# Optimization experiments

Hardware: AMD Instinct MI355X
Metric: run time of the kernel (lower is better)

Reference implementation:

```python
import jax, jax.numpy as jnp
import numpy as np

B, S, D = 4, 4096, 1024   # batch, seq_len, hidden_dim
E, K = 8, 2               # num_experts, num_experts_per_tok
H = 2 * D                 # expert MLP hidden dim


def setup_inputs() -> dict:
    key = jax.random.key(0)
    ks = jax.random.split(key, 4)
    sc = 0.02
    return {
        "hidden_states": jax.random.normal(ks[0], (B, S, D), jnp.float32),
        "Wr": (jax.random.normal(ks[1], (D, E), jnp.float32) * sc),
        "br": jnp.zeros((E,), jnp.float32),
        "W1": (jax.random.normal(ks[2], (E, D, H), jnp.float32) * sc),
        "b1": jnp.zeros((E, H), jnp.float32),
        "W2": (jax.random.normal(ks[3], (E, H, D), jnp.float32) * sc),
        "b2": jnp.zeros((E, D), jnp.float32),
    }


def reference(hidden_states, Wr, br, W1, b1, W2, b2):
    # Router: Linear -> Softmax (over experts), then top-k on the probabilities
    probs = jax.nn.softmax(hidden_states @ Wr + br, axis=-1)          # [B,S,E]
    top_w, top_i = jax.lax.top_k(probs, K)                            # [B,S,K]
    top_w = top_w / (top_w.sum(axis=-1, keepdims=True) + 1e-8)
    # Per-expert combine weight for every token (0 if expert not in top-k)
    combine = (jax.nn.one_hot(top_i, E, dtype=top_w.dtype)
               * top_w[..., None]).sum(axis=-2)                       # [B,S,E]
    # Reference semantics: run EVERY expert on EVERY token, then mask
    h = jnp.einsum('bsd,edh->ebsh', hidden_states, W1) + b1[:, None, None, :]  # [E,B,S,H]
    h = jax.nn.gelu(h, approximate=False)                             # exact GELU (torch default)
    expert_out = jnp.einsum('ebsh,ehd->ebsd', h, W2) + b2[:, None, None, :]    # [E,B,S,D]
    output = jnp.einsum('ebsd,bse->bsd', expert_out, combine)         # [B,S,D]
    return output
```

## Files before the change

kernel.cpp:

```cpp
#include <hip/hip_runtime.h>
#include <hip/hip_bf16.h>
#include <cstdint>
#include <cstddef>

#define TOKENS 16384
#define DIM    1024
#define NEXP   8
#define HID    2048
#define PAIRS  32768
#define PADCAP 33792
#define MTILES 264

typedef short     bf16x8 __attribute__((ext_vector_type(8)));
typedef float     f32x4  __attribute__((ext_vector_type(4)));

__device__ __forceinline__ unsigned short f2bf(float f) {
  union { float f; uint32_t u; } v; v.f = f;
  uint32_t u = v.u;
  uint32_t r = (u + 0x7FFFu + ((u >> 16) & 1u)) >> 16;
  return (unsigned short)r;
}

__device__ __forceinline__ void gload_lds16(const void* g, void* l) {
  __builtin_amdgcn_global_load_lds(
      (const __attribute__((address_space(1))) unsigned int*)g,
      (__attribute__((address_space(3))) unsigned int*)l,
      16, 0, 0);
}

__global__ __launch_bounds__(256) void tcvt(const float* __restrict__ src,
                                            unsigned short* __restrict__ dst,
                                            int R, int C) {
  __shared__ unsigned short t[64][72];
  const float* s = src + (size_t)blockIdx.z * R * C;
  unsigned short* d = dst + (size_t)blockIdx.z * R * C;
  int r0 = blockIdx.y * 64, c0 = blockIdx.x * 64;
  int tr = threadIdx.x >> 4;
  int tc = threadIdx.x & 15;
#pragma unroll
  for (int i = 0; i < 4; ++i) {
    int r = tr + i * 16;
    float4 v = *(const float4*)&s[(size_t)(r0 + r) * C + c0 + tc * 4];
    t[r][tc * 4 + 0] = f2bf(v.x);
    t[r][tc * 4 + 1] = f2bf(v.y);
    t[r][tc * 4 + 2] = f2bf(v.z);
    t[r][tc * 4 + 3] = f2bf(v.w);
  }
  __syncthreads();
#pragma unroll
  for (int i = 0; i < 4; ++i) {
    int c = tr + i * 16;
    ushort4 o;
    o.x = t[tc * 4 + 0][c];
    o.y = t[tc * 4 + 1][c];
    o.z = t[tc * 4 + 2][c];
    o.w = t[tc * 4 + 3][c];
    *(ushort4*)&d[(size_t)(c0 + c) * R + r0 + tc * 4] = o;
  }
}

__global__ __launch_bounds__(256) void router(const float* __restrict__ hs,
                                              const float* __restrict__ Wr,
                                              const float* __restrict__ br,
                                              unsigned short* __restrict__ Xb,
                                              int2* __restrict__ tok_e,
                                              float2* __restrict__ tok_w,
                                              int* __restrict__ counts) {
  __shared__ float wrT[NEXP][1032];
  __shared__ int hist[NEXP];
  int tid = threadIdx.x;
  if (tid < NEXP) hist[tid] = 0;
#pragma unroll
  for (int j = 0; j < 4; ++j) {
    int d = tid * 4 + j;
    float4 lo = *(const float4*)&Wr[d * 8];
    float4 hi = *(const float4*)&Wr[d * 8 + 4];
    wrT[0][d] = lo.x; wrT[1][d] = lo.y; wrT[2][d] = lo.z; wrT[3][d] = lo.w;
    wrT[4][d] = hi.x; wrT[5][d] = hi.y; wrT[6][d] = hi.z; wrT[7][d] = hi.w;
  }
  __syncthreads();
  int wave = tid >> 6, lane = tid & 63;

  for (int i = 0; i < 4; ++i) {
    int t = blockIdx.x * 16 + wave * 4 + i;
    float4 x[4];
#pragma unroll
    for (int p = 0; p < 4; ++p) {
      int d = p * 256 + lane * 4;
      x[p] = *(const float4*)&hs[(size_t)t * DIM + d];
      ushort4 o;
      o.x = f2bf(x[p].x); o.y = f2bf(x[p].y); o.z = f2bf(x[p].z); o.w = f2bf(x[p].w);
      *(ushort4*)&Xb[(size_t)t * DIM + d] = o;
    }
    float acc[NEXP];
#pragma unroll
    for (int e = 0; e < NEXP; ++e) {
      float a = 0.f;
#pragma unroll
      for (int p = 0; p < 4; ++p) {
        float4 w4 = *(const float4*)&wrT[e][p * 256 + lane * 4];
        a += x[p].x * w4.x + x[p].y * w4.y + x[p].z * w4.z + x[p].w * w4.w;
      }
      acc[e] = a;
    }
#pragma unroll
    for (int e = 0; e < NEXP; ++e) {
#pragma unroll
      for (int off = 32; off; off >>= 1) acc[e] += __shfl_xor(acc[e], off);
    }
    if (lane == 0) {
      float l[NEXP];
#pragma unroll
      for (int e = 0; e < NEXP; ++e) l[e] = acc[e] + br[e];
      float m = l[0];
#pragma unroll
      for (int e = 1; e < NEXP; ++e) m = fmaxf(m, l[e]);
      float p[NEXP], s = 0.f;
#pragma unroll
      for (int e = 0; e < NEXP; ++e) { p[e] = expf(l[e] - m); s += p[e]; }
      int e0 = 0;
#pragma unroll
      for (int e = 1; e < NEXP; ++e) if (p[e] > p[e0]) e0 = e;
      int e1 = (e0 == 0) ? 1 : 0;
#pragma unroll
      for (int e = 0; e < NEXP; ++e) if (e != e0 && p[e] > p[e1]) e1 = e;
      float q0 = p[e0] / s, q1 = p[e1] / s;
      float den = q0 + q1 + 1e-8f;
      tok_e[t] = make_int2(e0, e1);
      tok_w[t] = make_float2(q0 / den, q1 / den);
      atomicAdd(&hist[e0], 1);
      atomicAdd(&hist[e1], 1);
    }
  }
  __syncthreads();
  if (tid < NEXP)
    atomicAdd(&counts[(tid * 8 + (blockIdx.x & 7)) * 32], hist[tid]);
}

__global__ void mk_offsets(const int* __restrict__ counts, int* __restrict__ offs) {
  __shared__ int tot[NEXP];
  int e = threadIdx.x;
  if (e < NEXP) {
    int c = 0;
#pragma unroll
    for (int p = 0; p < 8; ++p) c += counts[(e * 8 + p) * 32];
    tot[e] = c;
  }
  __syncthreads();
  if (threadIdx.x == 0) {
    int o = 0;
#pragma unroll
    for (int i = 0; i < NEXP; ++i) {
      offs[i] = o;
      o += (tot[i] + 127) & ~127;
    }
    offs[NEXP] = o;
  }
}

__global__ __launch_bounds__(256) void scatter(const int2* __restrict__ tok_e,
                                               const float2* __restrict__ tok_w,
                                               const int* __restrict__ offs,
                                               int* __restrict__ gfill,
                                               int* __restrict__ ptok,
                                               float* __restrict__ pw) {
  __shared__ int lfill[NEXP], lbase[NEXP];
  int tid = threadIdx.x;
  if (tid < NEXP) lfill[tid] = 0;
  __syncthreads();
  int t = blockIdx.x * 256 + tid;
  int2 e = tok_e[t];
  float2 w = tok_w[t];
  int r0 = atomicAdd(&lfill[e.x], 1);
  int r1 = atomicAdd(&lfill[e.y], 1);
  __syncthreads();
  if (tid < NEXP) lbase[tid] = atomicAdd(&gfill[tid * 32], lfill[tid]);
  __syncthreads();
  int p0 = offs[e.x] + lbase[e.x] + r0;
  ptok[p0] = t; pw[p0] = w.x;
  int p1 = offs[e.y] + lbase[e.y] + r1;
  ptok[p1] = t; pw[p1] = w.y;
}

template <int MODE>
__global__ __launch_bounds__(256) void gemm_moe(
    const unsigned short* __restrict__ Asrc,
    const unsigned short* __restrict__ Bsrc,
    const float* __restrict__ bias,
    const int* __restrict__ offs,
    const int* __restrict__ ptok,
    const float* __restrict__ pw,
    unsigned short* __restrict__ Abuf,
    float* __restrict__ Out,
    int Ktot, int Ntot) {
  int row0 = blockIdx.x * 128;
  int padded_total = offs[NEXP];
  if (row0 >= padded_total) return;
  int e = 0;
  while (e < NEXP - 1 && row0 >= offs[e + 1]) ++e;
  int col0 = blockIdx.y * 128;

  __shared__ unsigned short As[128 * 64];
  __shared__ unsigned short Bs[128 * 64];
  __shared__ int   sTok[128];
  __shared__ float sW[128];

  int tid = threadIdx.x, wave = tid >> 6, lane = tid & 63;

  if (MODE == 1 && tid < 128) {
    sTok[tid] = ptok[row0 + tid];
    sW[tid]   = pw[row0 + tid];
  }

  int swz_src = (((lane & 7) ^ ((lane >> 3) & 7)) << 4);
  const char* aBase[4];
  const char* bBase[4];
#pragma unroll
  for (int i = 0; i < 4; ++i) {
    int r = wave * 32 + i * 8 + (lane >> 3);
    long arow;
    if (MODE == 0) arow = ptok[row0 + r];
    else           arow = row0 + r;
    aBase[i] = (const char*)Asrc + (size_t)arow * Ktot * 2 + swz_src;
    bBase[i] = (const char*)Bsrc + ((size_t)e * Ntot + col0 + r) * Ktot * 2 + swz_src;
  }

  f32x4 acc[4][4] = {};

  int wm = wave >> 1, wn = wave & 1;
  int rsel = lane & 15;
  int kblk = (lane >> 4) * 16;
  int rswz = (lane & 7) << 4;

  for (int kt = 0; kt < Ktot; kt += 64) {
    __syncthreads();
#pragma unroll
    for (int i = 0; i < 4; ++i) {
      gload_lds16(aBase[i] + kt * 2, &As[(wave * 32 + i * 8) * 64]);
      gload_lds16(bBase[i] + kt * 2, &Bs[(wave * 32 + i * 8) * 64]);
    }
    __syncthreads();
#pragma unroll
    for (int kk = 0; kk < 2; ++kk) {
      bf16x8 af[4], bfr[4];
#pragma unroll
      for (int i = 0; i < 4; ++i) {
        int row = wm * 64 + i * 16 + rsel;
        af[i] = *(const bf16x8*)((const char*)As + row * 128 + ((kk * 64 + kblk) ^ rswz));
      }
#pragma unroll
      for (int j = 0; j < 4; ++j) {
        int row = wn * 64 + j * 16 + rsel;
        bfr[j] = *(const bf16x8*)((const char*)Bs + row * 128 + ((kk * 64 + kblk) ^ rswz));
      }
#pragma unroll
      for (int i = 0; i < 4; ++i)
#pragma unroll
        for (int j = 0; j < 4; ++j)
          acc[i][j] = __builtin_amdgcn_mfma_f32_16x16x32_bf16(af[i], bfr[j], acc[i][j], 0, 0, 0);
    }
  }

  int crow = (lane >> 4) * 4;
  int ccol = lane & 15;
#pragma unroll
  for (int i = 0; i < 4; ++i) {
#pragma unroll
    for (int j = 0; j < 4; ++j) {
      int gcol = col0 + wn * 64 + j * 16 + ccol;
      float bv = bias[(size_t)e * Ntot + gcol];
#pragma unroll
      for (int r = 0; r < 4; ++r) {
        int lrow = wm * 64 + i * 16 + crow + r;
        float v = acc[i][j][r] + bv;
        if (MODE == 0) {
          float g = 0.5f * v * (1.0f + erff(v * 0.70710678118654752f));
          Abuf[(size_t)(row0 + lrow) * HID + gcol] = f2bf(g);
        } else {
          atomicAdd(&Out[(size_t)sTok[lrow] * DIM + gcol], sW[lrow] * v);
        }
      }
    }
  }
}

extern "C" void kernel_launch(void* const* d_in, const int* in_sizes, int n_in,
                              void* d_out, int out_size, void* d_ws, size_t ws_size,
                              hipStream_t stream) {
  const float* hs = (const float*)d_in[0];
  const float* Wr = (const float*)d_in[1];
  const float* br = (const float*)d_in[2];
  const float* W1 = (const float*)d_in[3];
  const float* b1 = (const float*)d_in[4];
  const float* W2 = (const float*)d_in[5];
  const float* b2 = (const float*)d_in[6];
  float* out = (float*)d_out;

  char* ws = (char*)d_ws;
  unsigned short* W1bT = (unsigned short*)(ws);
  unsigned short* W2bT = (unsigned short*)(ws + 33554432);
  unsigned short* Xb   = (unsigned short*)(ws + 67108864);
  unsigned short* Abuf = (unsigned short*)(ws + 100663296);
  char* rb = ws + 239075328;
  int*    counts = (int*)(rb);
  int*    gfill  = (int*)(rb + 8192);
  int*    offs   = (int*)(rb + 9216);
  int2*   tok_e  = (int2*)(rb + 9344);
  float2* tok_w  = (float2*)(rb + 140416);
  int*    ptok   = (int*)(rb + 271488);
  float*  pw     = (float*)(rb + 406656);
  size_t routing_bytes = 541824;

  hipMemsetAsync(rb, 0, routing_bytes, stream);
  hipMemsetAsync(out, 0, (size_t)out_size * sizeof(float), stream);

  dim3 t1g(HID / 64, DIM / 64, NEXP);
  tcvt<<<t1g, 256, 0, stream>>>(W1, W1bT, DIM, HID);
  dim3 t2g(DIM / 64, HID / 64, NEXP);
  tcvt<<<t2g, 256, 0, stream>>>(W2, W2bT, HID, DIM);

  router<<<1024, 256, 0, stream>>>(hs, Wr, br, Xb, tok_e, tok_w, counts);
  mk_offsets<<<1, 64, 0, stream>>>(counts, offs);
  scatter<<<TOKENS / 256, 256, 0, stream>>>(tok_e, tok_w, offs, gfill, ptok, pw);

  dim3 g1(MTILES, HID / 128);
  gemm_moe<0><<<g1, 256, 0, stream>>>(Xb, W1bT, b1, offs, ptok, pw, Abuf, out, DIM, HID);
  dim3 g2(MTILES, DIM / 128);
  gemm_moe<1><<<g2, 256, 0, stream>>>(Abuf, W2bT, b2, offs, ptok, pw, Abuf, out, HID, DIM);
}
```

Baseline: 817.2 us.

## Double-buffer LDS tiles in MoE GEMM and swap grid axes for locality

Adds a two-stage LDS ping-pong buffer so the global-to-LDS loads for the next K tile are issued before the MFMA work on the current tile. This drops one of the two barriers per iteration, hiding load latency behind compute. It also swaps the grid axes so consecutive blocks share the same row tile (A rows) across column tiles, which should improve L2 reuse of the gathered activations. LDS use doubles to 64KB per block, which may reduce occupancy. The barrier placement also relies on the async LDS loads having completed before the end-of-iteration barrier, since there is no explicit wait on the in-flight loads.

```diff
diff --git a/kernel.cpp b/kernel.cpp
--- a/kernel.cpp
+++ b/kernel.cpp
@@ -193,15 +193,15 @@
     unsigned short* __restrict__ Abuf,
     float* __restrict__ Out,
     int Ktot, int Ntot) {
-  int row0 = blockIdx.x * 128;
+  int row0 = blockIdx.y * 128;
   int padded_total = offs[NEXP];
   if (row0 >= padded_total) return;
   int e = 0;
   while (e < NEXP - 1 && row0 >= offs[e + 1]) ++e;
-  int col0 = blockIdx.y * 128;
-
-  __shared__ unsigned short As[128 * 64];
-  __shared__ unsigned short Bs[128 * 64];
+  int col0 = blockIdx.x * 128;
+
+  __shared__ unsigned short As[2][128 * 64];
+  __shared__ unsigned short Bs[2][128 * 64];
   __shared__ int   sTok[128];
   __shared__ float sW[128];
 
@@ -232,26 +232,35 @@
   int kblk = (lane >> 4) * 16;
   int rswz = (lane & 7) << 4;
 
-  for (int kt = 0; kt < Ktot; kt += 64) {
-    __syncthreads();
-#pragma unroll
-    for (int i = 0; i < 4; ++i) {
-      gload_lds16(aBase[i] + kt * 2, &As[(wave * 32 + i * 8) * 64]);
-      gload_lds16(bBase[i] + kt * 2, &Bs[(wave * 32 + i * 8) * 64]);
-    }
-    __syncthreads();
+#pragma unroll
+  for (int i = 0; i < 4; ++i) {
+    gload_lds16(aBase[i], &As[0][(wave * 32 + i * 8) * 64]);
+    gload_lds16(bBase[i], &Bs[0][(wave * 32 + i * 8) * 64]);
+  }
+  __syncthreads();
+
+  int cur = 0;
+  for (int kt = 0; kt < Ktot; kt += 64, cur ^= 1) {
+    if (kt + 64 < Ktot) {
+      int nxt = cur ^ 1;
+#pragma unroll
+      for (int i = 0; i < 4; ++i) {
+        gload_lds16(aBase[i] + (kt + 64) * 2, &As[nxt][(wave * 32 + i * 8) * 64]);
+        gload_lds16(bBase[i] + (kt + 64) * 2, &Bs[nxt][(wave * 32 + i * 8) * 64]);
+      }
+    }
 #pragma unroll
     for (int kk = 0; kk < 2; ++kk) {
       bf16x8 af[4], bfr[4];
 #pragma unroll
       for (int i = 0; i < 4; ++i) {
         int row = wm * 64 + i * 16 + rsel;
-        af[i] = *(const bf16x8*)((const char*)As + row * 128 + ((kk * 64 + kblk) ^ rswz));
+        af[i] = *(const bf16x8*)((const char*)As[cur] + row * 128 + ((kk * 64 + kblk) ^ rswz));
       }
 #pragma unroll
       for (int j = 0; j < 4; ++j) {
         int row = wn * 64 + j * 16 + rsel;
-        bfr[j] = *(const bf16x8*)((const char*)Bs + row * 128 + ((kk * 64 + kblk) ^ rswz));
+        bfr[j] = *(const bf16x8*)((const char*)Bs[cur] + row * 128 + ((kk * 64 + kblk) ^ rswz));
       }
 #pragma unroll
       for (int i = 0; i < 4; ++i)
@@ -259,6 +268,7 @@
         for (int j = 0; j < 4; ++j)
           acc[i][j] = __builtin_amdgcn_mfma_f32_16x16x32_bf16(af[i], bfr[j], acc[i][j], 0, 0, 0);
     }
+    __syncthreads();
   }
 
   int crow = (lane >> 4) * 4;
@@ -323,8 +333,8 @@
   mk_offsets<<<1, 64, 0, stream>>>(counts, offs);
   scatter<<<TOKENS / 256, 256, 0, stream>>>(tok_e, tok_w, offs, gfill, ptok, pw);
 
-  dim3 g1(MTILES, HID / 128);
+  dim3 g1(HID / 128, MTILES);
   gemm_moe<0><<<g1, 256, 0, stream>>>(Xb, W1bT, b1, offs, ptok, pw, Abuf, out, DIM, HID);
-  dim3 g2(MTILES, DIM / 128);
+  dim3 g2(DIM / 128, MTILES);
   gemm_moe<1><<<g2, 256, 0, stream>>>(Abuf, W2bT, b2, offs, ptok, pw, Abuf, out, HID, DIM);
 }
```

After: 827.2 us. No clear change (+1.2%).
